# Optimization experiments

Measured on AMD Instinct MI355X. Metric: run time of the kernel, lower is better.

## Reference

```python
import jax, jax.numpy as jnp
import numpy as np

HIDDEN = 768
NUM_HEADS = 12
HEAD_DIM = HIDDEN // NUM_HEADS
WINDOW = 128
NEG = -1e30  # stand-in for -inf that is safe under autodiff


def setup_inputs() -> dict:
    key = jax.random.key(0)
    ks = jax.random.split(key, 12)
    B, S = 2, 2048
    hidden = jax.random.normal(ks[0], (B, S, HIDDEN), dtype=jnp.float32)
    attention_mask = jnp.ones((B, S), dtype=jnp.int32)
    global_mask = jax.random.randint(ks[1], (B, S), 0, 2, dtype=jnp.int32)
    def lin(kw, kb):
        W = jax.random.normal(kw, (HIDDEN, HIDDEN), dtype=jnp.float32) * 0.02
        b = jax.random.normal(kb, (HIDDEN,), dtype=jnp.float32) * 0.02
        return W, b
    Wq, bq = lin(ks[2], ks[3])
    Wk, bk = lin(ks[4], ks[5])
    Wv, bv = lin(ks[6], ks[7])
    Wo, bo = lin(ks[8], ks[9])
    return {"hidden": hidden, "attention_mask": attention_mask, "global_mask": global_mask,
            "Wq": Wq, "bq": bq, "Wk": Wk, "bk": bk, "Wv": Wv, "bv": bv, "Wo": Wo, "bo": bo}


def _attend(hidden, attention_mask, global_mask, Wq, bq, Wk, bk, Wv, bv, Wo, bo):
    B, S, H = hidden.shape
    def proj(W, b):
        # (B,S,H) -> (B,nh,S,hd); nn.Linear computes x @ W.T + b
        return (hidden @ W.T + b).reshape(B, S, NUM_HEADS, HEAD_DIM).transpose(0, 2, 1, 3)
    q, k, v = proj(Wq, bq), proj(Wk, bk), proj(Wv, bv)
    scale = jnp.asarray(np.sqrt(HEAD_DIM), dtype=hidden.dtype)
    scores = jnp.einsum('bhqd,bhkd->bhqk', q, k) / scale  # (B,nh,S,S)
    # sliding window mask: |i-j| <= WINDOW
    idx = jnp.arange(S)
    window = (jnp.abs(idx[:, None] - idx[None, :]) <= WINDOW)  # (S,S)
    g = global_mask.astype(bool)
    combined = window[None] | g[:, :, None] | g[:, None, :]     # (B,S,S)
    combined = combined & attention_mask.astype(bool)[:, None, :]  # pad mask on keys
    scores = jnp.where(combined[:, None, :, :], scores, NEG)
    attn = jax.nn.softmax(scores, axis=-1)
    # torch code zeroes NaN rows (fully masked); replicate safely
    attn = jnp.where(jnp.isnan(attn), 0.0, attn)
    out = jnp.einsum('bhqk,bhkd->bhqd', attn, v)  # (B,nh,S,hd)
    out = out.transpose(0, 2, 1, 3).reshape(B, S, H)
    return out @ Wo.T + bo


def reference(hidden, attention_mask, global_mask, Wq, bq, Wk, bk, Wv, bv, Wo, bo):
    return _attend(hidden, attention_mask, global_mask, Wq, bq, Wk, bk, Wv, bv, Wo, bo)
```

## Files before the change

kernel.cpp:

```cpp
#include <hip/hip_runtime.h>
#include <math.h>

#define S_LEN 2048
#define HID   768
#define NH    12
#define HD    64
#define WIN   128
#define NEGV  (-1e30f)
#define QSCALE 0.1803368801111204f
#define NROW  49152

typedef __attribute__((ext_vector_type(8))) short short8v;
typedef __attribute__((ext_vector_type(4))) float float4v;
typedef unsigned short u16;

__device__ __forceinline__ u16 f2bf(float f) {
    union { float f; unsigned int u; } c; c.f = f;
    unsigned int u = c.u + 0x7FFFu + ((c.u >> 16) & 1u);
    return (u16)(u >> 16);
}

__device__ __forceinline__ short8v cvt8(float4 a, float4 b) {
    short8v t;
    t[0]=(short)f2bf(a.x); t[1]=(short)f2bf(a.y); t[2]=(short)f2bf(a.z); t[3]=(short)f2bf(a.w);
    t[4]=(short)f2bf(b.x); t[5]=(short)f2bf(b.y); t[6]=(short)f2bf(b.z); t[7]=(short)f2bf(b.w);
    return t;
}

__device__ __forceinline__ unsigned int pk2bf(float a, float b) {
    unsigned int r;
    asm("v_cvt_pk_bf16_f32 %0, %1, %2" : "=v"(r) : "v"(a), "v"(b));
    return r;
}

__device__ __forceinline__ float exp2_fast(float x) {
    float r;
    asm("v_exp_f32 %0, %1" : "=v"(r) : "v"(x));
    return r;
}

__device__ __forceinline__ short8v mk8(unsigned a, unsigned b, unsigned c, unsigned d) {
    union { short8v v; unsigned u[4]; } t;
    t.u[0]=a; t.u[1]=b; t.u[2]=c; t.u[3]=d; return t.v;
}

__device__ __forceinline__ float bf2f(u16 v) {
    union { float f; unsigned u; } c; c.u = ((unsigned)v) << 16; return c.f;
}

__device__ __forceinline__ void gload_lds16(const void* g, void* l) {
    __builtin_amdgcn_global_load_lds(
        (const __attribute__((address_space(1))) unsigned int*)g,
        (__attribute__((address_space(3))) unsigned int*)l, 16, 0, 0);
}

__global__ __launch_bounds__(256) void convert_inputs(
    const float* __restrict__ hidden, const float* __restrict__ Wq,
    const float* __restrict__ Wk, const float* __restrict__ Wv,
    const float* __restrict__ Wo, u16* __restrict__ hbf, u16* __restrict__ w4)
{
    const int y = blockIdx.y;
    const float* src; u16* dst; int n; float scale = 1.f;
    if (y == 0) { src = hidden; dst = hbf; n = 4096*HID; }
    else {
        src = (y==1) ? Wq : (y==2) ? Wk : (y==3) ? Wv : Wo;
        dst = w4 + (size_t)(y-1)*HID*HID;
        n = HID*HID;
        if (y == 1) scale = QSCALE;
    }
    const int idx = (blockIdx.x*256 + threadIdx.x) * 8;
    if (idx >= n) return;
    float4 f0 = *(const float4*)(src + idx);
    float4 f1 = *(const float4*)(src + idx + 4);
    f0.x*=scale; f0.y*=scale; f0.z*=scale; f0.w*=scale;
    f1.x*=scale; f1.y*=scale; f1.z*=scale; f1.w*=scale;
    *(short8v*)(dst + idx) = cvt8(f0, f1);
}

__global__ __launch_bounds__(256) void gemm_mfma(
    const u16* __restrict__ A, const u16* __restrict__ W4,
    const float* __restrict__ bA, const float* __restrict__ bB,
    const float* __restrict__ bC, u16* __restrict__ obf,
    u16* __restrict__ ovt, float* __restrict__ of32, int mode)
{
    __shared__ __align__(16) u16 As[128*32];
    __shared__ __align__(16) u16 Bs[128*32];

    const int tid = threadIdx.x;
    const int w = tid >> 6, l = tid & 63;
    const int lx = l & 15, lg = l >> 4;
    const int wr = w >> 1, wc = w & 1;
    const int m0 = blockIdx.x * 128, n0 = blockIdx.y * 128;
    const int z = (mode == 0) ? blockIdx.z : 3;
    const float* bias = (mode == 1) ? bA : (z == 0 ? bA : (z == 1 ? bB : bC));
    const float bscale = (mode == 0 && z == 0) ? QSCALE : 1.0f;
    const u16* Wp = W4 + (size_t)z * (HID*HID);

    float4v acc[4][4];
    const float4v fz = {0.f,0.f,0.f,0.f};
    #pragma unroll
    for (int i = 0; i < 4; i++)
        #pragma unroll
        for (int j = 0; j < 4; j++) acc[i][j] = fz;

    for (int kt = 0; kt < HID/32; kt++) {
        const int k0 = kt * 32;
        __syncthreads();
        #pragma unroll
        for (int rnd = 0; rnd < 2; rnd++) {
            const int ch  = rnd*256 + w*64 + l;
            const int row = ch >> 2, kc = ch & 3;
            gload_lds16(A  + (size_t)(m0+row)*HID + k0 + kc*8,
                        As + (size_t)(rnd*256 + w*64)*8);
            gload_lds16(Wp + (size_t)(n0+row)*HID + k0 + kc*8,
                        Bs + (size_t)(rnd*256 + w*64)*8);
        }
        __syncthreads();
        short8v af[4], bfr[4];
        #pragma unroll
        for (int i = 0; i < 4; i++) {
            af[i]  = *(const short8v*)(As + (wr*64 + i*16 + lx)*32 + lg*8);
            bfr[i] = *(const short8v*)(Bs + (wc*64 + i*16 + lx)*32 + lg*8);
        }
        #pragma unroll
        for (int i = 0; i < 4; i++)
            #pragma unroll
            for (int j = 0; j < 4; j++)
                acc[i][j] = __builtin_amdgcn_mfma_f32_16x16x32_bf16(af[i], bfr[j], acc[i][j], 0, 0, 0);
    }

    #pragma unroll
    for (int j = 0; j < 4; j++) {
        const int col = n0 + wc*64 + j*16 + lx;
        const float bval = bias[col] * bscale;
        const int hh = col >> 6, d = col & 63;
        #pragma unroll
        for (int i = 0; i < 4; i++) {
            const int rbase = m0 + wr*64 + i*16 + lg*4;
            const int bb = rbase >> 11, s = rbase & 2047;
            const float v0 = acc[i][j][0] + bval;
            const float v1 = acc[i][j][1] + bval;
            const float v2 = acc[i][j][2] + bval;
            const float v3 = acc[i][j][3] + bval;
            if (mode == 1) {
                of32[(size_t)(rbase+0)*HID + col] = v0;
                of32[(size_t)(rbase+1)*HID + col] = v1;
                of32[(size_t)(rbase+2)*HID + col] = v2;
                of32[(size_t)(rbase+3)*HID + col] = v3;
            } else if (z == 2) {
                uint2 ow; ow.x = pk2bf(v0, v1); ow.y = pk2bf(v2, v3);
                *(uint2*)&ovt[(((size_t)bb*NH + hh)*HD + d)*S_LEN + s] = ow;
            } else {
                u16* base = obf + (size_t)z * ((size_t)2*S_LEN*HID);
                base[(((size_t)bb*NH + hh)*S_LEN + s+0)*HD + d] = f2bf(v0);
                base[(((size_t)bb*NH + hh)*S_LEN + s+1)*HD + d] = f2bf(v1);
                base[(((size_t)bb*NH + hh)*S_LEN + s+2)*HD + d] = f2bf(v2);
                base[(((size_t)bb*NH + hh)*S_LEN + s+3)*HD + d] = f2bf(v3);
            }
        }
    }
}

__global__ __launch_bounds__(256) void attn_split(
    const u16* __restrict__ Q, const u16* __restrict__ K,
    const u16* __restrict__ Vt, const int* __restrict__ amask,
    const int* __restrict__ gmask, u16* __restrict__ O0,
    u16* __restrict__ O1, float* __restrict__ Mp, float* __restrict__ Lp)
{
    __shared__ __align__(16) u16 Ks[64*64];
    __shared__ __align__(16) u16 Vs[64*64];
    __shared__ __align__(16) float fA[64];
    __shared__ __align__(16) float fB[64];

    const int tid = threadIdx.x;
    const int w  = tid >> 6;
    const int l  = tid & 63;
    const int lx = l & 15;
    const int lg = l >> 4;

    const int bid = blockIdx.x;
    const int swz = (bid & 7) * 192 + (bid >> 3);
    const int half = swz & 1;
    const int q0 = ((swz >> 1) & 31) * 64;
    const int hb = swz >> 6;
    const int h  = hb % NH;
    const int b  = hb / NH;
    const size_t bh = ((size_t)b*NH + h) * S_LEN;

    const int q_glob = q0 + w*16 + lx;

    short8v aq[2];
    {
        const u16* qp = Q + (bh + q_glob)*HD + lg*8;
        aq[0] = *(const short8v*)(qp);
        aq[1] = *(const short8v*)(qp + 32);
    }
    const int gq = gmask[(size_t)b*S_LEN + q_glob];
    const float* fP = gq ? fA : fB;

    float m_i = NEGV, l_i = 0.f;
    float4v o_acc[4];
    const float4v fzv = {0.f, 0.f, 0.f, 0.f};
    #pragma unroll
    for (int db = 0; db < 4; db++) o_acc[db] = fzv;

    const int str = tid >> 2;
    const int stc = tid & 3;
    const int xr  = (str & 32) | (((str>>2)&1)<<4) | (((str>>4)&1)<<3)
                  | (((str>>3)&1)<<2) | (str & 3);
    const int rbK = xr * 128;
    const int swK = (xr & 7) << 4;
    const int rbV = str * 128;
    const int swV = (str & 7) << 4;
    const u16* Kbase = K + bh * HD;
    const u16* Vbase = Vt + (size_t)(b*NH + h) * HD * S_LEN;

    uint4 rk0, rk1, rv0, rv1;
    int ram = 0, rgk = 0;

#define STAGE_REGS(KT) do {                                                   \
    const int kk0_ = (KT) * 64;                                               \
    const u16* kp_ = Kbase + (size_t)(kk0_ + str)*HD + stc*16;                \
    rk0 = *(const uint4*)(kp_); rk1 = *(const uint4*)(kp_ + 8);               \
    const u16* vp_ = Vbase + (size_t)str*S_LEN + kk0_ + stc*16;               \
    rv0 = *(const uint4*)(vp_); rv1 = *(const uint4*)(vp_ + 8);               \
    if (tid < 64) {                                                           \
        ram = amask[(size_t)b*S_LEN + kk0_ + tid];                            \
        rgk = gmask[(size_t)b*S_LEN + kk0_ + tid];                            \
    }                                                                         \
} while(0)

#define WRITE_LDS() do {                                                      \
    *(uint4*)((char*)Ks + rbK + ((stc*32)      ^ swK)) = rk0;                 \
    *(uint4*)((char*)Ks + rbK + ((stc*32 + 16) ^ swK)) = rk1;                 \
    *(uint4*)((char*)Vs + rbV + ((stc*32)      ^ swV)) = rv0;                 \
    *(uint4*)((char*)Vs + rbV + ((stc*32 + 16) ^ swV)) = rv1;                 \
    if (tid < 64) {                                                           \
        fA[tid] = ram ? 0.f : NEGV;                                           \
        fB[tid] = (ram && rgk) ? 0.f : NEGV;                                  \
    }                                                                         \
} while(0)

#define COMPUTE(K0) do {                                                      \
       \
    float4v sacc[4];                                                          \
    const int adq_ = ((K0) > q0) ? ((K0) - q0) : (q0 - (K0));                 \
    if (adq_ <= 64) {                                                         \
        _Pragma("unroll")                                                     \
        for (int kb = 0; kb < 4; kb++) {                                      \
            const int base_ = 32*(kb>>1) + 8*lg + 4*(kb&1);                   \
            float4 fa4 = *(const float4*)&fA[base_];                          \
            sacc[kb][0]=fa4.x; sacc[kb][1]=fa4.y;                             \
            sacc[kb][2]=fa4.z; sacc[kb][3]=fa4.w;                             \
        }                                                                     \
    } else if (adq_ >= 192) {                                                 \
        _Pragma("unroll")                                                     \
        for (int kb = 0; kb < 4; kb++) {                                      \
            const int base_ = 32*(kb>>1) + 8*lg + 4*(kb&1);                   \
            float4 fp4 = *(const float4*)&fP[base_];                          \
            sacc[kb][0]=fp4.x; sacc[kb][1]=fp4.y;                             \
            sacc[kb][2]=fp4.z; sacc[kb][3]=fp4.w;                             \
        }                                                                     \
    } else {                                                                  \
        _Pragma("unroll")                                                     \
        for (int kb = 0; kb < 4; kb++) {                                      \
            const int base_ = 32*(kb>>1) + 8*lg + 4*(kb&1);                   \
            float4 fa4 = *(const float4*)&fA[base_];                          \
            float4 fb4 = *(const float4*)&fB[base_];                          \
            const int e_ = q_glob - ((K0) + base_);                           \
            _Pragma("unroll")                                                 \
            for (int r = 0; r < 4; r++) {                                     \
                int dd_ = e_ - r; dd_ = dd_ < 0 ? -dd_ : dd_;                 \
                const bool wing_ = (dd_ <= WIN) || gq;                        \
                sacc[kb][r] = wing_ ? (&fa4.x)[r] : (&fb4.x)[r];              \
            }                                                                 \
        }                                                                     \
    }                                                                         \
    __builtin_amdgcn_s_setprio(1);                                            \
    _Pragma("unroll")                                                         \
    for (int kb = 0; kb < 4; kb++) {                                          \
        const int row_ = kb*16 + lx;                                          \
        const int ksw_ = (row_ & 7) << 4;                                     \
        _Pragma("unroll")                                                     \
        for (int ks = 0; ks < 2; ks++) {                                      \
            short8v bk_ = *(const short8v*)((char*)Ks + row_*128 +            \
                                            ((16*lg + 64*ks) ^ ksw_));        \
            sacc[kb] = __builtin_amdgcn_mfma_f32_16x16x32_bf16(bk_, aq[ks],   \
                                                          sacc[kb], 0, 0, 0); \
        }                                                                     \
    }                                                                         \
    __builtin_amdgcn_s_setprio(0);                                            \
    float mloc;                                                               \
    {                                                                         \
        float t0 = fmaxf(fmaxf(sacc[0][0], sacc[0][1]), sacc[0][2]);          \
        float t1 = fmaxf(fmaxf(sacc[0][3], sacc[1][0]), sacc[1][1]);          \
        float t2 = fmaxf(fmaxf(sacc[1][2], sacc[1][3]), sacc[2][0]);          \
        float t3 = fmaxf(fmaxf(sacc[2][1], sacc[2][2]), sacc[2][3]);          \
        float t4 = fmaxf(fmaxf(sacc[3][0], sacc[3][1]), sacc[3][2]);          \
        mloc = fmaxf(fmaxf(fmaxf(t0, t1), t2),                                \
                     fmaxf(fmaxf(t3, t4), sacc[3][3]));                       \
    }                                                                         \
    mloc = fmaxf(mloc, __shfl_xor(mloc, 16));                                 \
    mloc = fmaxf(mloc, __shfl_xor(mloc, 32));                                 \
    if (__any(mloc > m_i + 8.0f)) {                                           \
        const float mnew_ = fmaxf(m_i, mloc);                                 \
        const float sc_ = exp2_fast(m_i - mnew_);                             \
        l_i *= sc_;                                                           \
        _Pragma("unroll")                                                     \
        for (int db = 0; db < 4; db++)                                        \
            _Pragma("unroll")                                                 \
            for (int r = 0; r < 4; r++) o_acc[db][r] *= sc_;                  \
        m_i = mnew_;                                                          \
    }                                                                         \
    float p[4][4];                                                            \
    _Pragma("unroll")                                                         \
    for (int kb = 0; kb < 4; kb++)                                            \
        _Pragma("unroll")                                                     \
        for (int r = 0; r < 4; r++)                                           \
            p[kb][r] = exp2_fast(sacc[kb][r] - m_i);                          \
    {                                                                         \
        float s0 = (p[0][0]+p[0][1]) + (p[0][2]+p[0][3]);                     \
        float s1 = (p[1][0]+p[1][1]) + (p[1][2]+p[1][3]);                     \
        float s2 = (p[2][0]+p[2][1]) + (p[2][2]+p[2][3]);                     \
        float s3 = (p[3][0]+p[3][1]) + (p[3][2]+p[3][3]);                     \
        float lsum = (s0+s1) + (s2+s3);                                       \
        lsum += __shfl_xor(lsum, 16);                                         \
        lsum += __shfl_xor(lsum, 32);                                         \
        l_i += lsum;                                                          \
    }                                                                         \
      \
    __builtin_amdgcn_s_setprio(1);                                            \
    _Pragma("unroll")                                                         \
    for (int hh = 0; hh < 2; hh++) {                                          \
        short8v pa_ = mk8(pk2bf(p[2*hh][0],   p[2*hh][1]),                    \
                          pk2bf(p[2*hh][2],   p[2*hh][3]),                    \
                          pk2bf(p[2*hh+1][0], p[2*hh+1][1]),                  \
                          pk2bf(p[2*hh+1][2], p[2*hh+1][3]));                 \
        _Pragma("unroll")                                                     \
        for (int db = 0; db < 4; db++) {                                      \
            const int drow_ = db*16 + lx;                                     \
            short8v bv_ = *(const short8v*)((char*)Vs + drow_*128 +           \
                                    ((16*lg + 64*hh) ^ ((drow_ & 7) << 4)));  \
            o_acc[db] = __builtin_amdgcn_mfma_f32_16x16x32_bf16(bv_, pa_,     \
                                                          o_acc[db], 0, 0, 0);\
        }                                                                     \
    }                                                                         \
    __builtin_amdgcn_s_setprio(0);                                            \
} while(0)

    const int t0 = half * 16, t1 = t0 + 16;
    STAGE_REGS(t0);
    WRITE_LDS();
    __syncthreads();

    for (int kt = t0; kt < t1; kt++) {
        const int kn = (kt+1 < t1) ? (kt+1) : kt;
        STAGE_REGS(kn);
        COMPUTE(kt*64);
        __syncthreads();
        WRITE_LDS();
        __syncthreads();
    }

#undef STAGE_REGS
#undef WRITE_LDS
#undef COMPUTE

    {
        u16* op = (half ? O1 : O0) + (bh + q_glob)*HD + lg*4;
        #pragma unroll
        for (int db = 0; db < 4; db++) {
            uint2 ow;
            ow.x = pk2bf(o_acc[db][0], o_acc[db][1]);
            ow.y = pk2bf(o_acc[db][2], o_acc[db][3]);
            *(uint2*)(op + db*16) = ow;
        }
        if (lg == 0) {
            Mp[half*NROW + bh + q_glob] = m_i;
            Lp[half*NROW + bh + q_glob] = l_i;
        }
    }
}

__global__ __launch_bounds__(256) void attn_merge(
    const u16* __restrict__ O0, const u16* __restrict__ O1,
    const float* __restrict__ Mp, const float* __restrict__ Lp,
    u16* __restrict__ AO)
{
    const int idx8 = (blockIdx.x*256 + threadIdx.x) * 8;
    const int b   = idx8 / (S_LEN*HID);
    const int rem = idx8 - b*(S_LEN*HID);
    const int s   = rem / HID;
    const int hd  = rem - s*HID;
    const int hh  = hd >> 6;
    const int d0  = hd & 63;
    const int row = (b*NH + hh)*S_LEN + s;

    const float m0 = Mp[row], m1 = Mp[NROW + row];
    const float l0 = Lp[row], l1 = Lp[NROW + row];
    const float m  = fmaxf(m0, m1);
    const float w0 = exp2_fast(m0 - m);
    const float w1 = exp2_fast(m1 - m);
    const float inv = 1.f / (l0*w0 + l1*w1);

    const size_t ioff = (size_t)row*HD + d0;
    uint4 a = *(const uint4*)(O0 + ioff);
    uint4 c = *(const uint4*)(O1 + ioff);
    const u16* ap = (const u16*)&a;
    const u16* cp = (const u16*)&c;
    unsigned ow[4];
    #pragma unroll
    for (int j = 0; j < 4; j++) {
        float f0 = (bf2f(ap[2*j])*w0   + bf2f(cp[2*j])*w1)   * inv;
        float f1 = (bf2f(ap[2*j+1])*w0 + bf2f(cp[2*j+1])*w1) * inv;
        ow[j] = pk2bf(f0, f1);
    }
    uint4 o; o.x=ow[0]; o.y=ow[1]; o.z=ow[2]; o.w=ow[3];
    *(uint4*)(AO + idx8) = o;
}

extern "C" void kernel_launch(void* const* d_in, const int* in_sizes, int n_in,
                              void* d_out, int out_size, void* d_ws, size_t ws_size,
                              hipStream_t stream)
{
    const float* hidden = (const float*)d_in[0];
    const int*   amask  = (const int*)d_in[1];
    const int*   gmask  = (const int*)d_in[2];
    const float* Wq = (const float*)d_in[3];
    const float* bq = (const float*)d_in[4];
    const float* Wk = (const float*)d_in[5];
    const float* bk = (const float*)d_in[6];
    const float* Wv = (const float*)d_in[7];
    const float* bv = (const float*)d_in[8];
    const float* Wo = (const float*)d_in[9];
    const float* bo = (const float*)d_in[10];
    float* out = (float*)d_out;

    char* ws = (char*)d_ws;
    const size_t NTOK = (size_t)2 * S_LEN * HID;
    u16* hbf   = (u16*)(ws);
    u16* w4    = (u16*)(ws + 6291456);
    float* Mp  = (float*)(ws + 6291456);
    float* Lp  = Mp + 2*NROW;
    u16* qkvbf = (u16*)(ws + 11010048);
    u16* vtbf  = (u16*)(ws + 29884416);
    u16* aobf  = (u16*)(ws + 36175872);

    convert_inputs<<<dim3(1536, 5), 256, 0, stream>>>(hidden, Wq, Wk, Wv, Wo, hbf, w4);

    gemm_mfma<<<dim3(32, 6, 3), 256, 0, stream>>>(hbf, w4, bq, bk, bv, qkvbf, vtbf, nullptr, 0);

    u16* Qbf = qkvbf;
    u16* Kbf = qkvbf + NTOK;

    attn_split<<<dim3(1536), 256, 0, stream>>>(Qbf, Kbf, vtbf, amask, gmask,
                                               aobf, hbf, Mp, Lp);

    attn_merge<<<dim3(1536), 256, 0, stream>>>(aobf, hbf, Mp, Lp, vtbf);

    gemm_mfma<<<dim3(32, 6), 256, 0, stream>>>(vtbf, w4, bo, nullptr, nullptr, nullptr, nullptr, out, 1);
}
```

Baseline: 112.5 us.

## Switch attention to 32x32x16 MFMA with 128-query tiles and precomputed mask biases

The attention kernel moves from 16x16x32 to 32x32x16 bf16 MFMA. Each block now covers 128 queries (32 per wave), so the grid halves to 768 blocks. K and V are stored in LDS in an MFMA-operand layout, and P is routed through a per-wave LDS buffer to re-form it as a B operand. Per-key mask bias arrays are built once in the convert kernel instead of per tile in LDS. This aims to cut K/V reload traffic and instruction overhead per FLOP, but adds LDS traffic for P, more register pressure (launch_bounds 256,3), and fewer blocks.

```diff
diff --git a/kernel.cpp b/kernel.cpp
--- a/kernel.cpp
+++ b/kernel.cpp
@@ -11,7 +11,7 @@
 #define NROW  49152
 
 typedef __attribute__((ext_vector_type(8))) short short8v;
-typedef __attribute__((ext_vector_type(4))) float float4v;
+typedef __attribute__((ext_vector_type(16))) float f32x16;
 typedef unsigned short u16;
 
 __device__ __forceinline__ u16 f2bf(float f) {
@@ -39,11 +39,6 @@
     return r;
 }
 
-__device__ __forceinline__ short8v mk8(unsigned a, unsigned b, unsigned c, unsigned d) {
-    union { short8v v; unsigned u[4]; } t;
-    t.u[0]=a; t.u[1]=b; t.u[2]=c; t.u[3]=d; return t.v;
-}
-
 __device__ __forceinline__ float bf2f(u16 v) {
     union { float f; unsigned u; } c; c.u = ((unsigned)v) << 16; return c.f;
 }
@@ -54,12 +49,46 @@
         (__attribute__((address_space(3))) unsigned int*)l, 16, 0, 0);
 }
 
+__device__ __forceinline__ void cinit_uni(f32x16& S, const float* src) {
+    #pragma unroll
+    for (int m = 0; m < 4; m++) {
+        float4 f = *(const float4*)(src + 8*m);
+        S[4*m+0]=f.x; S[4*m+1]=f.y; S[4*m+2]=f.z; S[4*m+3]=f.w;
+    }
+}
+__device__ __forceinline__ void cinit_mixed(f32x16& S, const float* fa, const float* fb,
+                                            int ebase, int gq) {
+    #pragma unroll
+    for (int m = 0; m < 4; m++) {
+        float4 a = *(const float4*)(fa + 8*m);
+        float4 b = *(const float4*)(fb + 8*m);
+        const int e = ebase - 8*m;
+        S[4*m+0] = (gq || (unsigned)(e     + 128) <= 256u) ? a.x : b.x;
+        S[4*m+1] = (gq || (unsigned)(e - 1 + 128) <= 256u) ? a.y : b.y;
+        S[4*m+2] = (gq || (unsigned)(e - 2 + 128) <= 256u) ? a.z : b.z;
+        S[4*m+3] = (gq || (unsigned)(e - 3 + 128) <= 256u) ? a.w : b.w;
+    }
+}
+
 __global__ __launch_bounds__(256) void convert_inputs(
     const float* __restrict__ hidden, const float* __restrict__ Wq,
     const float* __restrict__ Wk, const float* __restrict__ Wv,
-    const float* __restrict__ Wo, u16* __restrict__ hbf, u16* __restrict__ w4)
+    const float* __restrict__ Wo, const int* __restrict__ amask,
+    const int* __restrict__ gmask, u16* __restrict__ hbf,
+    u16* __restrict__ w4, float* __restrict__ fAg, float* __restrict__ fBg)
 {
     const int y = blockIdx.y;
+    if (y == 5) {
+        const int idx = (blockIdx.x*256 + threadIdx.x) * 8;
+        if (idx >= 2*S_LEN) return;
+        #pragma unroll
+        for (int u = 0; u < 8; u++) {
+            const int am = amask[idx+u], gk = gmask[idx+u];
+            fAg[idx+u] = am ? 0.f : NEGV;
+            fBg[idx+u] = (am && gk) ? 0.f : NEGV;
+        }
+        return;
+    }
     const float* src; u16* dst; int n; float scale = 1.f;
     if (y == 0) { src = hidden; dst = hbf; n = 4096*HID; }
     else {
@@ -77,6 +106,7 @@
     *(short8v*)(dst + idx) = cvt8(f0, f1);
 }
 
+typedef __attribute__((ext_vector_type(4))) float float4v;
 __global__ __launch_bounds__(256) void gemm_mfma(
     const u16* __restrict__ A, const u16* __restrict__ W4,
     const float* __restrict__ bA, const float* __restrict__ bB,
@@ -161,62 +191,60 @@
     }
 }
 
-__global__ __launch_bounds__(256) void attn_split(
+__global__ __launch_bounds__(256, 3) void attn_split(
     const u16* __restrict__ Q, const u16* __restrict__ K,
-    const u16* __restrict__ Vt, const int* __restrict__ amask,
-    const int* __restrict__ gmask, u16* __restrict__ O0,
-    u16* __restrict__ O1, float* __restrict__ Mp, float* __restrict__ Lp)
+    const u16* __restrict__ Vt, const float* __restrict__ fAg,
+    const float* __restrict__ fBg, const int* __restrict__ gmask,
+    u16* __restrict__ O0, u16* __restrict__ O1,
+    float* __restrict__ Mp, float* __restrict__ Lp)
 {
-    __shared__ __align__(16) u16 Ks[64*64];
-    __shared__ __align__(16) u16 Vs[64*64];
-    __shared__ __align__(16) float fA[64];
-    __shared__ __align__(16) float fB[64];
+    __shared__ __align__(16) u16 Ks[8*64*8];
+    __shared__ __align__(16) u16 Vs[8*64*8];
+    __shared__ __align__(16) u16 Ps[4*2048];
 
     const int tid = threadIdx.x;
-    const int w  = tid >> 6;
-    const int l  = tid & 63;
-    const int lx = l & 15;
-    const int lg = l >> 4;
+    const int w   = tid >> 6;
+    const int l   = tid & 63;
+    const int hi  = l >> 5;
+    const int ln31 = l & 31;
 
     const int bid = blockIdx.x;
-    const int swz = (bid & 7) * 192 + (bid >> 3);
+    const int swz = (bid & 7) * 96 + (bid >> 3);
     const int half = swz & 1;
-    const int q0 = ((swz >> 1) & 31) * 64;
-    const int hb = swz >> 6;
-    const int h  = hb % NH;
-    const int b  = hb / NH;
+    const int q0  = ((swz >> 1) & 15) * 128;
+    const int hb  = swz >> 5;
+    const int h   = hb % NH;
+    const int b   = hb / NH;
     const size_t bh = ((size_t)b*NH + h) * S_LEN;
 
-    const int q_glob = q0 + w*16 + lx;
-
-    short8v aq[2];
+    const int q_glob = q0 + 32*w + ln31;
+
+    short8v aq[4];
     {
-        const u16* qp = Q + (bh + q_glob)*HD + lg*8;
+        const u16* qp = Q + (bh + q_glob)*HD + 8*hi;
         aq[0] = *(const short8v*)(qp);
-        aq[1] = *(const short8v*)(qp + 32);
+        aq[1] = *(const short8v*)(qp + 16);
+        aq[2] = *(const short8v*)(qp + 32);
+        aq[3] = *(const short8v*)(qp + 48);
     }
     const int gq = gmask[(size_t)b*S_LEN + q_glob];
-    const float* fP = gq ? fA : fB;
+    const float* fAb_ = fAg + (size_t)b*S_LEN;
+    const float* fBb_ = fBg + (size_t)b*S_LEN;
+    const float* fPb_ = gq ? fAb_ : fBb_;
 
     float m_i = NEGV, l_i = 0.f;
-    float4v o_acc[4];
-    const float4v fzv = {0.f, 0.f, 0.f, 0.f};
-    #pragma unroll
-    for (int db = 0; db < 4; db++) o_acc[db] = fzv;
+    f32x16 oa0, oa1;
+    #pragma unroll
+    for (int i = 0; i < 16; i++) { oa0[i] = 0.f; oa1[i] = 0.f; }
 
     const int str = tid >> 2;
     const int stc = tid & 3;
-    const int xr  = (str & 32) | (((str>>2)&1)<<4) | (((str>>4)&1)<<3)
-                  | (((str>>3)&1)<<2) | (str & 3);
-    const int rbK = xr * 128;
-    const int swK = (xr & 7) << 4;
-    const int rbV = str * 128;
-    const int swV = (str & 7) << 4;
+    const int wbase = ((str >> 5)*4 + stc)*512 + (str & 31)*8;
     const u16* Kbase = K + bh * HD;
     const u16* Vbase = Vt + (size_t)(b*NH + h) * HD * S_LEN;
+    char* Pb = (char*)(Ps + w*2048);
 
     uint4 rk0, rk1, rv0, rv1;
-    int ram = 0, rgk = 0;
 
 #define STAGE_REGS(KT) do {                                                   \
     const int kk0_ = (KT) * 64;                                               \
@@ -224,126 +252,98 @@
     rk0 = *(const uint4*)(kp_); rk1 = *(const uint4*)(kp_ + 8);               \
     const u16* vp_ = Vbase + (size_t)str*S_LEN + kk0_ + stc*16;               \
     rv0 = *(const uint4*)(vp_); rv1 = *(const uint4*)(vp_ + 8);               \
-    if (tid < 64) {                                                           \
-        ram = amask[(size_t)b*S_LEN + kk0_ + tid];                            \
-        rgk = gmask[(size_t)b*S_LEN + kk0_ + tid];                            \
-    }                                                                         \
 } while(0)
 
 #define WRITE_LDS() do {                                                      \
-    *(uint4*)((char*)Ks + rbK + ((stc*32)      ^ swK)) = rk0;                 \
-    *(uint4*)((char*)Ks + rbK + ((stc*32 + 16) ^ swK)) = rk1;                 \
-    *(uint4*)((char*)Vs + rbV + ((stc*32)      ^ swV)) = rv0;                 \
-    *(uint4*)((char*)Vs + rbV + ((stc*32 + 16) ^ swV)) = rv1;                 \
-    if (tid < 64) {                                                           \
-        fA[tid] = ram ? 0.f : NEGV;                                           \
-        fB[tid] = (ram && rgk) ? 0.f : NEGV;                                  \
-    }                                                                         \
+    *(uint4*)(Ks + wbase)       = rk0;                                        \
+    *(uint4*)(Ks + wbase + 256) = rk1;                                        \
+    *(uint4*)(Vs + wbase)       = rv0;                                        \
+    *(uint4*)(Vs + wbase + 256) = rv1;                                        \
 } while(0)
 
 #define COMPUTE(K0) do {                                                      \
-       \
-    float4v sacc[4];                                                          \
-    const int adq_ = ((K0) > q0) ? ((K0) - q0) : (q0 - (K0));                 \
-    if (adq_ <= 64) {                                                         \
-        _Pragma("unroll")                                                     \
-        for (int kb = 0; kb < 4; kb++) {                                      \
-            const int base_ = 32*(kb>>1) + 8*lg + 4*(kb&1);                   \
-            float4 fa4 = *(const float4*)&fA[base_];                          \
-            sacc[kb][0]=fa4.x; sacc[kb][1]=fa4.y;                             \
-            sacc[kb][2]=fa4.z; sacc[kb][3]=fa4.w;                             \
-        }                                                                     \
-    } else if (adq_ >= 192) {                                                 \
-        _Pragma("unroll")                                                     \
-        for (int kb = 0; kb < 4; kb++) {                                      \
-            const int base_ = 32*(kb>>1) + 8*lg + 4*(kb&1);                   \
-            float4 fp4 = *(const float4*)&fP[base_];                          \
-            sacc[kb][0]=fp4.x; sacc[kb][1]=fp4.y;                             \
-            sacc[kb][2]=fp4.z; sacc[kb][3]=fp4.w;                             \
-        }                                                                     \
+    f32x16 s0, s1;                                                            \
+    const int diff_ = (K0) - q0;                                              \
+    if (diff_ == 0 || diff_ == 64) {                                          \
+        cinit_uni(s0, fAb_ + (K0) + 4*hi);                                    \
+        cinit_uni(s1, fAb_ + (K0) + 32 + 4*hi);                               \
+    } else if (diff_ >= 256 || diff_ <= -192) {                               \
+        cinit_uni(s0, fPb_ + (K0) + 4*hi);                                    \
+        cinit_uni(s1, fPb_ + (K0) + 32 + 4*hi);                               \
     } else {                                                                  \
-        _Pragma("unroll")                                                     \
-        for (int kb = 0; kb < 4; kb++) {                                      \
-            const int base_ = 32*(kb>>1) + 8*lg + 4*(kb&1);                   \
-            float4 fa4 = *(const float4*)&fA[base_];                          \
-            float4 fb4 = *(const float4*)&fB[base_];                          \
-            const int e_ = q_glob - ((K0) + base_);                           \
-            _Pragma("unroll")                                                 \
-            for (int r = 0; r < 4; r++) {                                     \
-                int dd_ = e_ - r; dd_ = dd_ < 0 ? -dd_ : dd_;                 \
-                const bool wing_ = (dd_ <= WIN) || gq;                        \
-                sacc[kb][r] = wing_ ? (&fa4.x)[r] : (&fb4.x)[r];              \
-            }                                                                 \
-        }                                                                     \
+        cinit_mixed(s0, fAb_ + (K0) + 4*hi, fBb_ + (K0) + 4*hi,               \
+                    q_glob - ((K0) + 4*hi), gq);                              \
+        cinit_mixed(s1, fAb_ + (K0) + 32 + 4*hi, fBb_ + (K0) + 32 + 4*hi,     \
+                    q_glob - ((K0) + 32 + 4*hi), gq);                         \
     }                                                                         \
     __builtin_amdgcn_s_setprio(1);                                            \
     _Pragma("unroll")                                                         \
-    for (int kb = 0; kb < 4; kb++) {                                          \
-        const int row_ = kb*16 + lx;                                          \
-        const int ksw_ = (row_ & 7) << 4;                                     \
-        _Pragma("unroll")                                                     \
-        for (int ks = 0; ks < 2; ks++) {                                      \
-            short8v bk_ = *(const short8v*)((char*)Ks + row_*128 +            \
-                                            ((16*lg + 64*ks) ^ ksw_));        \
-            sacc[kb] = __builtin_amdgcn_mfma_f32_16x16x32_bf16(bk_, aq[ks],   \
-                                                          sacc[kb], 0, 0, 0); \
-        }                                                                     \
+    for (int dd = 0; dd < 4; dd++) {                                          \
+        short8v ak0 = *(const short8v*)(Ks + dd*512 + l*8);                   \
+        short8v ak1 = *(const short8v*)(Ks + (4+dd)*512 + l*8);               \
+        s0 = __builtin_amdgcn_mfma_f32_32x32x16_bf16(ak0, aq[dd], s0, 0,0,0); \
+        s1 = __builtin_amdgcn_mfma_f32_32x32x16_bf16(ak1, aq[dd], s1, 0,0,0); \
     }                                                                         \
     __builtin_amdgcn_s_setprio(0);                                            \
-    float mloc;                                                               \
-    {                                                                         \
-        float t0 = fmaxf(fmaxf(sacc[0][0], sacc[0][1]), sacc[0][2]);          \
-        float t1 = fmaxf(fmaxf(sacc[0][3], sacc[1][0]), sacc[1][1]);          \
-        float t2 = fmaxf(fmaxf(sacc[1][2], sacc[1][3]), sacc[2][0]);          \
-        float t3 = fmaxf(fmaxf(sacc[2][1], sacc[2][2]), sacc[2][3]);          \
-        float t4 = fmaxf(fmaxf(sacc[3][0], sacc[3][1]), sacc[3][2]);          \
-        mloc = fmaxf(fmaxf(fmaxf(t0, t1), t2),                                \
-                     fmaxf(fmaxf(t3, t4), sacc[3][3]));                       \
-    }                                                                         \
-    mloc = fmaxf(mloc, __shfl_xor(mloc, 16));                                 \
+    float mx0 = fmaxf(s0[0], s1[0]), mx1 = fmaxf(s0[1], s1[1]);               \
+    float mx2 = fmaxf(s0[2], s1[2]), mx3 = fmaxf(s0[3], s1[3]);               \
+    _Pragma("unroll")                                                         \
+    for (int i = 4; i < 16; i += 4) {                                         \
+        mx0 = fmaxf(mx0, fmaxf(s0[i],   s1[i]));                              \
+        mx1 = fmaxf(mx1, fmaxf(s0[i+1], s1[i+1]));                            \
+        mx2 = fmaxf(mx2, fmaxf(s0[i+2], s1[i+2]));                            \
+        mx3 = fmaxf(mx3, fmaxf(s0[i+3], s1[i+3]));                            \
+    }                                                                         \
+    float mloc = fmaxf(fmaxf(mx0, mx1), fmaxf(mx2, mx3));                     \
     mloc = fmaxf(mloc, __shfl_xor(mloc, 32));                                 \
     if (__any(mloc > m_i + 8.0f)) {                                           \
         const float mnew_ = fmaxf(m_i, mloc);                                 \
         const float sc_ = exp2_fast(m_i - mnew_);                             \
         l_i *= sc_;                                                           \
         _Pragma("unroll")                                                     \
-        for (int db = 0; db < 4; db++)                                        \
-            _Pragma("unroll")                                                 \
-            for (int r = 0; r < 4; r++) o_acc[db][r] *= sc_;                  \
+        for (int i = 0; i < 16; i++) { oa0[i] *= sc_; oa1[i] *= sc_; }        \
         m_i = mnew_;                                                          \
     }                                                                         \
-    float p[4][4];                                                            \
     _Pragma("unroll")                                                         \
-    for (int kb = 0; kb < 4; kb++)                                            \
-        _Pragma("unroll")                                                     \
-        for (int r = 0; r < 4; r++)                                           \
-            p[kb][r] = exp2_fast(sacc[kb][r] - m_i);                          \
+    for (int i = 0; i < 16; i++) {                                            \
+        s0[i] = exp2_fast(s0[i] - m_i);                                       \
+        s1[i] = exp2_fast(s1[i] - m_i);                                       \
+    }                                                                         \
     {                                                                         \
-        float s0 = (p[0][0]+p[0][1]) + (p[0][2]+p[0][3]);                     \
-        float s1 = (p[1][0]+p[1][1]) + (p[1][2]+p[1][3]);                     \
-        float s2 = (p[2][0]+p[2][1]) + (p[2][2]+p[2][3]);                     \
-        float s3 = (p[3][0]+p[3][1]) + (p[3][2]+p[3][3]);                     \
-        float lsum = (s0+s1) + (s2+s3);                                       \
-        lsum += __shfl_xor(lsum, 16);                                         \
+        float a0 = (s0[0]+s0[1]) + (s0[2]+s0[3]);                             \
+        float a1 = (s0[4]+s0[5]) + (s0[6]+s0[7]);                             \
+        float a2 = (s0[8]+s0[9]) + (s0[10]+s0[11]);                           \
+        float a3 = (s0[12]+s0[13]) + (s0[14]+s0[15]);                         \
+        float b0 = (s1[0]+s1[1]) + (s1[2]+s1[3]);                             \
+        float b1 = (s1[4]+s1[5]) + (s1[6]+s1[7]);                             \
+        float b2 = (s1[8]+s1[9]) + (s1[10]+s1[11]);                           \
+        float b3 = (s1[12]+s1[13]) + (s1[14]+s1[15]);                         \
+        float lsum = ((a0+a1)+(a2+a3)) + ((b0+b1)+(b2+b3));                   \
         lsum += __shfl_xor(lsum, 32);                                         \
         l_i += lsum;                                                          \
     }                                                                         \
-      \
+    \
+    \
+    \
+    _Pragma("unroll")                                                         \
+    for (int g = 0; g < 4; g++) {                                             \
+        uint2 v0, v1;                                                         \
+        v0.x = pk2bf(s0[4*g+0], s0[4*g+1]);                                   \
+        v0.y = pk2bf(s0[4*g+2], s0[4*g+3]);                                   \
+        v1.x = pk2bf(s1[4*g+0], s1[4*g+1]);                                   \
+        v1.y = pk2bf(s1[4*g+2], s1[4*g+3]);                                   \
+        const int g0_ = g, g1_ = g + 4;                                       \
+        *(uint2*)(Pb + (g0_>>1)*1024 + (((g0_&1)<<5) | ln31)*16 + hi*8) = v0; \
+        *(uint2*)(Pb + (g1_>>1)*1024 + (((g1_&1)<<5) | ln31)*16 + hi*8) = v1; \
+    }                                                                         \
     __builtin_amdgcn_s_setprio(1);                                            \
     _Pragma("unroll")                                                         \
-    for (int hh = 0; hh < 2; hh++) {                                          \
-        short8v pa_ = mk8(pk2bf(p[2*hh][0],   p[2*hh][1]),                    \
-                          pk2bf(p[2*hh][2],   p[2*hh][3]),                    \
-                          pk2bf(p[2*hh+1][0], p[2*hh+1][1]),                  \
-                          pk2bf(p[2*hh+1][2], p[2*hh+1][3]));                 \
-        _Pragma("unroll")                                                     \
-        for (int db = 0; db < 4; db++) {                                      \
-            const int drow_ = db*16 + lx;                                     \
-            short8v bv_ = *(const short8v*)((char*)Vs + drow_*128 +           \
-                                    ((16*lg + 64*hh) ^ ((drow_ & 7) << 4)));  \
-            o_acc[db] = __builtin_amdgcn_mfma_f32_16x16x32_bf16(bv_, pa_,     \
-                                                          o_acc[db], 0, 0, 0);\
-        }                                                                     \
+    for (int c = 0; c < 4; c++) {                                             \
+        short8v pb  = *(const short8v*)(Pb + c*1024 + l*16);                  \
+        short8v av0 = *(const short8v*)(Vs + c*512 + l*8);                    \
+        short8v av1 = *(const short8v*)(Vs + (4+c)*512 + l*8);                \
+        oa0 = __builtin_amdgcn_mfma_f32_32x32x16_bf16(av0, pb, oa0, 0,0,0);   \
+        oa1 = __builtin_amdgcn_mfma_f32_32x32x16_bf16(av1, pb, oa1, 0,0,0);   \
     }                                                                         \
     __builtin_amdgcn_s_setprio(0);                                            \
 } while(0)
@@ -367,15 +367,15 @@
 #undef COMPUTE
 
     {
-        u16* op = (half ? O1 : O0) + (bh + q_glob)*HD + lg*4;
-        #pragma unroll
-        for (int db = 0; db < 4; db++) {
-            uint2 ow;
-            ow.x = pk2bf(o_acc[db][0], o_acc[db][1]);
-            ow.y = pk2bf(o_acc[db][2], o_acc[db][3]);
-            *(uint2*)(op + db*16) = ow;
-        }
-        if (lg == 0) {
+        u16* op = (half ? O1 : O0) + (bh + q_glob)*HD + 4*hi;
+        #pragma unroll
+        for (int m = 0; m < 4; m++) {
+            *(unsigned*)(op + 8*m)          = pk2bf(oa0[4*m],   oa0[4*m+1]);
+            *(unsigned*)(op + 8*m + 2)      = pk2bf(oa0[4*m+2], oa0[4*m+3]);
+            *(unsigned*)(op + 32 + 8*m)     = pk2bf(oa1[4*m],   oa1[4*m+1]);
+            *(unsigned*)(op + 32 + 8*m + 2) = pk2bf(oa1[4*m+2], oa1[4*m+3]);
+        }
+        if (l < 32) {
             Mp[half*NROW + bh + q_glob] = m_i;
             Lp[half*NROW + bh + q_glob] = l_i;
         }
@@ -443,18 +443,21 @@
     float* Mp  = (float*)(ws + 6291456);
     float* Lp  = Mp + 2*NROW;
     u16* qkvbf = (u16*)(ws + 11010048);
+    float* fAg = (float*)(ws + 23592960);
+    float* fBg = (float*)(ws + 23609344);
     u16* vtbf  = (u16*)(ws + 29884416);
     u16* aobf  = (u16*)(ws + 36175872);
 
-    convert_inputs<<<dim3(1536, 5), 256, 0, stream>>>(hidden, Wq, Wk, Wv, Wo, hbf, w4);
+    convert_inputs<<<dim3(1536, 6), 256, 0, stream>>>(
+        hidden, Wq, Wk, Wv, Wo, amask, gmask, hbf, w4, fAg, fBg);
 
     gemm_mfma<<<dim3(32, 6, 3), 256, 0, stream>>>(hbf, w4, bq, bk, bv, qkvbf, vtbf, nullptr, 0);
 
     u16* Qbf = qkvbf;
     u16* Kbf = qkvbf + NTOK;
 
-    attn_split<<<dim3(1536), 256, 0, stream>>>(Qbf, Kbf, vtbf, amask, gmask,
-                                               aobf, hbf, Mp, Lp);
+    attn_split<<<dim3(768), 256, 0, stream>>>(Qbf, Kbf, vtbf, fAg, fBg, gmask,
+                                              aobf, hbf, Mp, Lp);
 
     attn_merge<<<dim3(1536), 256, 0, stream>>>(aobf, hbf, Mp, Lp, vtbf);
 
```

Measured after the change: 113.8 us. Within noise of the previous version (+1.2%).
